# Kernel tuning notes

Hardware: AMD Instinct MI355X
Metric: run time of the kernel (lower is better)

The kernel has to match this reference:

```python
import jax, jax.numpy as jnp
import numpy as np

LN_EPS = 1e-5

def setup_inputs() -> dict:
    key = jax.random.key(0)
    k1, k2, k3, k4 = jax.random.split(key, 4)
    B, N, D, E = 2, 50000, 128, 800000
    H = jax.random.normal(k1, (B, N, D), dtype=jnp.float32)
    src = jax.random.randint(k2, (E,), 0, N, dtype=jnp.int64)
    dst = jax.random.randint(k3, (E,), 0, N, dtype=jnp.int64)
    W = jax.random.normal(k4, (D, D), dtype=jnp.float32) * (1.0 / np.sqrt(D))
    gamma = jnp.ones((D,), dtype=jnp.float32)
    beta = jnp.zeros((D,), dtype=jnp.float32)
    return {"H": H, "src": src, "dst": dst, "W": W, "gamma": gamma, "beta": beta}

def reference(H, src, dst, W, gamma, beta):
    # m = Linear(H) (no bias): [B,N,D]
    m = jnp.einsum('bnd,de->bne', H, W)
    # gather messages at src, scatter-add into dst along node dim
    agg = jnp.zeros_like(m).at[:, dst, :].add(m[:, src, :])
    x = H + jax.nn.gelu(agg, approximate=False)
    # LayerNorm over last dim
    mu = jnp.mean(x, axis=-1, keepdims=True)
    var = jnp.var(x, axis=-1, keepdims=True)
    return (x - mu) * jax.lax.rsqrt(var + LN_EPS) * gamma + beta
```

## Files before the change

kernel.cpp:

```cpp
#include <hip/hip_runtime.h>
#include <math.h>

#define DIM 128
#define LN_EPS 1e-5f
#define CAP 64
#define TPW 2

typedef unsigned short bf16_t;
typedef unsigned short u16;
typedef __attribute__((ext_vector_type(8))) short bf16x8;
typedef __attribute__((ext_vector_type(4))) float f32x4;

__device__ __forceinline__ bf16_t f2bf(float f) {
    unsigned u = __builtin_bit_cast(unsigned, f);
    u += 0x7FFFu + ((u >> 16) & 1u);
    return (bf16_t)(u >> 16);
}
__device__ __forceinline__ float bf2f(bf16_t h) {
    unsigned u = ((unsigned)h) << 16;
    return __builtin_bit_cast(float, u);
}

__global__ __launch_bounds__(256) void prep_kernel(
    const float* __restrict__ W, bf16_t* __restrict__ WT,
    int* __restrict__ cursor, int N)
{
    const int tid = blockIdx.x * 256 + threadIdx.x;
    if (tid < N) cursor[tid] = 0;
    if (tid < (DIM * DIM / 4)) {
        const float4 w = ((const float4*)W)[tid];
        const int k  = tid >> 5;
        const int n0 = (tid & 31) * 4;
        WT[(n0 + 0) * DIM + k] = f2bf(w.x);
        WT[(n0 + 1) * DIM + k] = f2bf(w.y);
        WT[(n0 + 2) * DIM + k] = f2bf(w.z);
        WT[(n0 + 3) * DIM + k] = f2bf(w.w);
    }
}

__global__ __launch_bounds__(256) void fill_kernel(
    const int* __restrict__ src, const int* __restrict__ dst,
    int* __restrict__ cursor, u16* __restrict__ eidxT, int N, int E)
{
    int e = blockIdx.x * 256 + threadIdx.x;
    if (e < E) {
        int d = dst[e];
        int pos = atomicAdd(&cursor[d], 1);
        if (pos < CAP) eidxT[(size_t)pos * N + d] = (u16)src[e];
    }
}

__global__ __launch_bounds__(256) void gemm_kernel(
    const float* __restrict__ Hmat, const bf16_t* __restrict__ WT,
    bf16_t* __restrict__ Mout, int nrows, int N)
{
    const int tid  = threadIdx.x;
    const int wave = tid >> 6;
    const int lane = tid & 63;
    const int quad = lane >> 4;
    const int l15  = lane & 15;

    bf16x8 wf[32];
    #pragma unroll
    for (int t = 0; t < 8; ++t)
        #pragma unroll
        for (int ks = 0; ks < 4; ++ks)
            wf[t * 4 + ks] = *(const bf16x8*)
                &WT[(size_t)(t * 16 + l15) * DIM + ks * 32 + quad * 8];

    const int baserow = (blockIdx.x * 4 + wave) * (TPW * 16);

    #pragma unroll
    for (int rt = 0; rt < TPW; ++rt) {
        const int arow = baserow + rt * 16 + l15;
        const float* Arow = Hmat + (size_t)((arow < nrows) ? arow : 0) * DIM;

        f32x4 acc[8];
        #pragma unroll
        for (int t = 0; t < 8; ++t) acc[t] = (f32x4){0.f, 0.f, 0.f, 0.f};

        #pragma unroll
        for (int ks = 0; ks < 4; ++ks) {
            const int k0 = ks * 32 + quad * 8;
            float4 a0 = *(const float4*)&Arow[k0];
            float4 a1 = *(const float4*)&Arow[k0 + 4];
            bf16x8 hf;
            hf[0] = (short)f2bf(a0.x); hf[1] = (short)f2bf(a0.y);
            hf[2] = (short)f2bf(a0.z); hf[3] = (short)f2bf(a0.w);
            hf[4] = (short)f2bf(a1.x); hf[5] = (short)f2bf(a1.y);
            hf[6] = (short)f2bf(a1.z); hf[7] = (short)f2bf(a1.w);

            #pragma unroll
            for (int t = 0; t < 8; ++t)
                acc[t] = __builtin_amdgcn_mfma_f32_16x16x32_bf16(
                             wf[t * 4 + ks], hf, acc[t], 0, 0, 0);
        }

        if (arow < nrows) {
            const int b = (arow >= N) ? 1 : 0;
            const int n = arow - (b ? N : 0);
            bf16_t* orow = Mout + ((size_t)n * 2 + b) * DIM;
            #pragma unroll
            for (int t = 0; t < 8; ++t) {
                ushort4 o;
                o.x = f2bf(acc[t][0]); o.y = f2bf(acc[t][1]);
                o.z = f2bf(acc[t][2]); o.w = f2bf(acc[t][3]);
                *(ushort4*)&orow[t * 16 + quad * 4] = o;
            }
        }
    }
}

__global__ __launch_bounds__(256) void gather_kernel(
    const bf16_t* __restrict__ M, const float* __restrict__ Hmat,
    const int* __restrict__ cursor, const u16* __restrict__ eidxT,
    const float* __restrict__ gamma, const float* __restrict__ beta,
    float* __restrict__ out, int N)
{
    const int wave = threadIdx.x >> 6;
    const int lane = threadIdx.x & 63;
    const int node = blockIdx.x * 4 + wave;
    if (node >= N) return;

    const int b  = lane >> 5;
    const int c4 = lane & 31;

    int cnt = cursor[node];
    if (cnt > CAP) cnt = CAP;

    int myidx = (lane < cnt) ? (int)eidxT[(size_t)lane * N + node] : 0;

    const ushort4* M4 = (const ushort4*)M;

    float acc0 = 0.f, acc1 = 0.f, acc2 = 0.f, acc3 = 0.f;
    int j = 0;
    for (; j + 8 <= cnt; j += 8) {
        ushort4 v[8];
        #pragma unroll
        for (int q = 0; q < 8; ++q) {
            int s = __shfl(myidx, j + q, 64);
            v[q] = M4[(size_t)s * 64 + lane];
        }
        #pragma unroll
        for (int q = 0; q < 8; ++q) {
            acc0 += bf2f(v[q].x); acc1 += bf2f(v[q].y);
            acc2 += bf2f(v[q].z); acc3 += bf2f(v[q].w);
        }
    }
    for (; j < cnt; ++j) {
        int s = __shfl(myidx, j, 64);
        ushort4 v0 = M4[(size_t)s * 64 + lane];
        acc0 += bf2f(v0.x); acc1 += bf2f(v0.y);
        acc2 += bf2f(v0.z); acc3 += bf2f(v0.w);
    }

    const size_t elembase = ((size_t)b * N + node) * DIM + c4 * 4;
    float4 h = *(const float4*)&Hmat[elembase];
    const float inv_sqrt2 = 0.70710678118654752f;
    float x0 = h.x + 0.5f * acc0 * (1.f + erff(acc0 * inv_sqrt2));
    float x1 = h.y + 0.5f * acc1 * (1.f + erff(acc1 * inv_sqrt2));
    float x2 = h.z + 0.5f * acc2 * (1.f + erff(acc2 * inv_sqrt2));
    float x3 = h.w + 0.5f * acc3 * (1.f + erff(acc3 * inv_sqrt2));

    float s  = x0 + x1 + x2 + x3;
    float ss = x0 * x0 + x1 * x1 + x2 * x2 + x3 * x3;
    #pragma unroll
    for (int o = 16; o > 0; o >>= 1) {
        s  += __shfl_xor(s,  o, 64);
        ss += __shfl_xor(ss, o, 64);
    }
    const float mean = s * (1.f / DIM);
    const float var  = ss * (1.f / DIM) - mean * mean;
    const float inv  = rsqrtf(var + LN_EPS);

    float4 gm = *(const float4*)&gamma[c4 * 4];
    float4 bt = *(const float4*)&beta[c4 * 4];
    float4 o;
    o.x = (x0 - mean) * inv * gm.x + bt.x;
    o.y = (x1 - mean) * inv * gm.y + bt.y;
    o.z = (x2 - mean) * inv * gm.z + bt.z;
    o.w = (x3 - mean) * inv * gm.w + bt.w;
    *(float4*)&out[elembase] = o;
}

extern "C" void kernel_launch(void* const* d_in, const int* in_sizes, int n_in,
                              void* d_out, int out_size, void* d_ws, size_t ws_size,
                              hipStream_t stream)
{
    const float* H     = (const float*)d_in[0];
    const int*   src   = (const int*)  d_in[1];
    const int*   dst   = (const int*)  d_in[2];
    const float* W     = (const float*)d_in[3];
    const float* gamma = (const float*)d_in[4];
    const float* beta  = (const float*)d_in[5];
    float* out = (float*)d_out;

    const int E     = in_sizes[1];
    const int total = in_sizes[0];
    const int nrows = total / DIM;
    const int N     = nrows / 2;

    char* ws = (char*)d_ws;
    bf16_t* Mbuf = (bf16_t*)ws;   ws += (size_t)total * sizeof(bf16_t);
    int* cursor  = (int*)ws;      ws += (size_t)N * sizeof(int);
    u16* eidxT   = (u16*)ws;      ws += (size_t)CAP * N * sizeof(u16);
    bf16_t* WT   = (bf16_t*)ws;   ws += (size_t)DIM * DIM * sizeof(bf16_t);

    int prep_elems = (N > DIM * DIM / 4) ? N : DIM * DIM / 4;
    prep_kernel<<<(prep_elems + 255) / 256, 256, 0, stream>>>(W, WT, cursor, N);

    fill_kernel<<<(E + 255) / 256, 256, 0, stream>>>(src, dst, cursor, eidxT, N, E);

    const int ROWS_PER_BLOCK = 4 * TPW * 16;
    gemm_kernel<<<(nrows + ROWS_PER_BLOCK - 1) / ROWS_PER_BLOCK, 256, 0, stream>>>(
        H, WT, Mbuf, nrows, N);

    gather_kernel<<<(N + 3) / 4, 256, 0, stream>>>(Mbuf, H, cursor, eidxT,
                                                   gamma, beta, out, N);
}
```

Before: 232.4 us.

## Fuse edge-bucket fill into GEMM launch and vectorize edge loads

Merges the independent edge-bucketing kernel and the bf16 MFMA GEMM into one launch, where the first FB blocks fill edge buckets and the rest compute the GEMM, so both run concurrently instead of back to back. The fill path now handles four edges per thread with int4 loads of dst and src. The gather kernel swaps __shfl for readlane so the source index becomes a scalar broadcast. Fused blocks share one register budget via launch_bounds(256,2), which may limit GEMM occupancy, and the int4 loads assume 16-byte-aligned index arrays.

```diff
diff --git a/kernel.cpp b/kernel.cpp
--- a/kernel.cpp
+++ b/kernel.cpp
@@ -38,22 +38,36 @@
     }
 }
 
-__global__ __launch_bounds__(256) void fill_kernel(
+__global__ __launch_bounds__(256, 2) void gemm_fill_kernel(
+    const float* __restrict__ Hmat, const bf16_t* __restrict__ WT,
+    bf16_t* __restrict__ Mout,
     const int* __restrict__ src, const int* __restrict__ dst,
-    int* __restrict__ cursor, u16* __restrict__ eidxT, int N, int E)
-{
-    int e = blockIdx.x * 256 + threadIdx.x;
-    if (e < E) {
-        int d = dst[e];
-        int pos = atomicAdd(&cursor[d], 1);
-        if (pos < CAP) eidxT[(size_t)pos * N + d] = (u16)src[e];
-    }
-}
-
-__global__ __launch_bounds__(256) void gemm_kernel(
-    const float* __restrict__ Hmat, const bf16_t* __restrict__ WT,
-    bf16_t* __restrict__ Mout, int nrows, int N)
-{
+    int* __restrict__ cursor, u16* __restrict__ eidxT,
+    int nrows, int N, int E, int FB)
+{
+    if ((int)blockIdx.x < FB) {
+        const int base = (blockIdx.x * 256 + threadIdx.x) * 4;
+        if (base + 3 < E) {
+            int4 d4 = *(const int4*)&dst[base];
+            int4 s4 = *(const int4*)&src[base];
+            int p0 = atomicAdd(&cursor[d4.x], 1);
+            int p1 = atomicAdd(&cursor[d4.y], 1);
+            int p2 = atomicAdd(&cursor[d4.z], 1);
+            int p3 = atomicAdd(&cursor[d4.w], 1);
+            if (p0 < CAP) eidxT[(size_t)p0 * N + d4.x] = (u16)s4.x;
+            if (p1 < CAP) eidxT[(size_t)p1 * N + d4.y] = (u16)s4.y;
+            if (p2 < CAP) eidxT[(size_t)p2 * N + d4.z] = (u16)s4.z;
+            if (p3 < CAP) eidxT[(size_t)p3 * N + d4.w] = (u16)s4.w;
+        } else {
+            for (int e = base; e < E; ++e) {
+                int d = dst[e];
+                int pos = atomicAdd(&cursor[d], 1);
+                if (pos < CAP) eidxT[(size_t)pos * N + d] = (u16)src[e];
+            }
+        }
+        return;
+    }
+
     const int tid  = threadIdx.x;
     const int wave = tid >> 6;
     const int lane = tid & 63;
@@ -68,7 +82,8 @@
             wf[t * 4 + ks] = *(const bf16x8*)
                 &WT[(size_t)(t * 16 + l15) * DIM + ks * 32 + quad * 8];
 
-    const int baserow = (blockIdx.x * 4 + wave) * (TPW * 16);
+    const int gblock  = blockIdx.x - FB;
+    const int baserow = (gblock * 4 + wave) * (TPW * 16);
 
     #pragma unroll
     for (int rt = 0; rt < TPW; ++rt) {
@@ -138,8 +153,8 @@
         ushort4 v[8];
         #pragma unroll
         for (int q = 0; q < 8; ++q) {
-            int s = __shfl(myidx, j + q, 64);
-            v[q] = M4[(size_t)s * 64 + lane];
+            int s = __builtin_amdgcn_readlane(myidx, j + q);
+            v[q] = (M4 + ((size_t)s << 6))[lane];
         }
         #pragma unroll
         for (int q = 0; q < 8; ++q) {
@@ -148,8 +163,8 @@
         }
     }
     for (; j < cnt; ++j) {
-        int s = __shfl(myidx, j, 64);
-        ushort4 v0 = M4[(size_t)s * 64 + lane];
+        int s = __builtin_amdgcn_readlane(myidx, j);
+        ushort4 v0 = (M4 + ((size_t)s << 6))[lane];
         acc0 += bf2f(v0.x); acc1 += bf2f(v0.y);
         acc2 += bf2f(v0.z); acc3 += bf2f(v0.w);
     }
@@ -209,11 +224,11 @@
     int prep_elems = (N > DIM * DIM / 4) ? N : DIM * DIM / 4;
     prep_kernel<<<(prep_elems + 255) / 256, 256, 0, stream>>>(W, WT, cursor, N);
 
-    fill_kernel<<<(E + 255) / 256, 256, 0, stream>>>(src, dst, cursor, eidxT, N, E);
-
+    const int FB = (E + 1023) / 1024;
     const int ROWS_PER_BLOCK = 4 * TPW * 16;
-    gemm_kernel<<<(nrows + ROWS_PER_BLOCK - 1) / ROWS_PER_BLOCK, 256, 0, stream>>>(
-        H, WT, Mbuf, nrows, N);
+    const int GB = (nrows + ROWS_PER_BLOCK - 1) / ROWS_PER_BLOCK;
+    gemm_fill_kernel<<<FB + GB, 256, 0, stream>>>(H, WT, Mbuf, src, dst,
+                                                  cursor, eidxT, nrows, N, E, FB);
 
     gather_kernel<<<(N + 3) / 4, 256, 0, stream>>>(Mbuf, H, cursor, eidxT,
                                                    gamma, beta, out, N);
```

Result: faster. 225.9 us (-2.8%).
